# Optimization experiments

Hardware: AMD Instinct MI355X
Metric: run time of the kernel (lower is better)

Reference implementation:

```python
import jax, jax.numpy as jnp
import numpy as np

SEQ_LEN = 512
MAX_SPAN = 15
BATCH = 8
HIDDEN = 1024
WIDTH_DIM = 64
NUM_LABELS = 3


def _enumerate_spans(seq_len, max_span):
    starts, ends = [], []
    for s in range(seq_len):
        for e in range(s, min(s + max_span, seq_len)):
            starts.append(s)
            ends.append(e)
    return np.asarray(starts, np.int32), np.asarray(ends, np.int32)


def setup_inputs() -> dict:
    key = jax.random.key(0)
    k = jax.random.split(key, 6)
    starts, ends = _enumerate_spans(SEQ_LEN, MAX_SPAN)  # N = 7575
    d_in = HIDDEN * 2 + WIDTH_DIM  # 2112
    return {
        "sequence_output": jax.random.normal(k[0], (BATCH, SEQ_LEN, HIDDEN), jnp.float32),
        "width_emb": jax.random.normal(k[1], (MAX_SPAN, WIDTH_DIM), jnp.float32) * 0.02,
        "W1": jax.random.normal(k[2], (d_in, HIDDEN), jnp.float32) * (1.0 / np.sqrt(d_in)),
        "b1": jnp.zeros((HIDDEN,), jnp.float32),
        "W2": jax.random.normal(k[3], (HIDDEN, NUM_LABELS), jnp.float32) * (1.0 / np.sqrt(HIDDEN)),
        "b2": jnp.zeros((NUM_LABELS,), jnp.float32),
        "span_starts": jnp.asarray(starts),
        "span_ends": jnp.asarray(ends),
    }


def reference(sequence_output, width_emb, W1, b1, W2, b2, span_starts, span_ends):
    # Gather start/end token representations for every candidate span.
    B = sequence_output.shape[0]
    N = span_starts.shape[0]
    start_repr = sequence_output[:, span_starts]            # [B, N, H]
    end_repr = sequence_output[:, span_ends]                # [B, N, H]
    width_repr = width_emb[span_ends - span_starts]         # [N, 64]
    width_repr = jnp.broadcast_to(width_repr[None], (B, N, width_repr.shape[-1]))
    span_reprs = jnp.concatenate([start_repr, end_repr, width_repr], axis=-1)  # [B, N, 2H+64]
    # Span classifier MLP (dropout is identity in eval mode).
    h = jax.nn.relu(jnp.einsum("bnd,dh->bnh", span_reprs, W1) + b1)
    logits = jnp.einsum("bnh,hl->bnl", h, W2) + b2          # [B, N, num_labels]
    return logits
```

## Files before the change

### kernel.cpp

```cpp
#include <hip/hip_runtime.h>
#include <stdint.h>

#define SEQ 512
#define BATCH 8
#define HID 1024

typedef __attribute__((ext_vector_type(8))) __bf16 bf16x8;
typedef __attribute__((ext_vector_type(4))) float f32x4;
typedef __attribute__((ext_vector_type(2))) float f32x2;

__device__ __forceinline__ unsigned short f2bf(float f) {
    unsigned int u = __float_as_uint(f);
    unsigned int r = 0x7fffu + ((u >> 16) & 1u);
    return (unsigned short)((u + r) >> 16);
}

__device__ __forceinline__ f32x2 up2(unsigned int v) {
    f32x2 r;
    r.x = __uint_as_float(v << 16);
    r.y = __uint_as_float(v & 0xffff0000u);
    return r;
}

template <int CTRL>
__device__ __forceinline__ float dpp_add(float x) {
    int t = __builtin_amdgcn_update_dpp(0, __float_as_int(x), CTRL, 0xf, 0xf, true);
    return x + __int_as_float(t);
}
__device__ __forceinline__ float wave_sum63(float x) {
    x = dpp_add<0x111>(x);
    x = dpp_add<0x112>(x);
    x = dpp_add<0x114>(x);
    x = dpp_add<0x118>(x);
    x = dpp_add<0x142>(x);
    x = dpp_add<0x143>(x);
    return x;
}

__global__ __launch_bounds__(256) void k_prep(const float* __restrict__ seq,
                                              const float* __restrict__ W1,
                                              ushort* __restrict__ seqb,
                                              ushort* __restrict__ Bt) {
    __shared__ float tile[32][33];
    const int bid = blockIdx.x;
    const int tid = threadIdx.x;
    if (bid < 4096) {
        int i = bid * 256 + tid;
        float4 v = ((const float4*)seq)[i];
        ushort4 o;
        o.x = f2bf(v.x); o.y = f2bf(v.y); o.z = f2bf(v.z); o.w = f2bf(v.w);
        ((ushort4*)seqb)[i] = o;
    } else {
        int idx = bid - 4096;
        int nb = (idx & 63) * 32, kb = (idx >> 6) * 32;
        int tx = tid & 31, ty = tid >> 5;
        int n = nb + tx;
        int rb = (n < 1024) ? 0 : 1024;
        int nc = n - rb;
#pragma unroll
        for (int i = 0; i < 4; ++i) {
            int k = kb + ty + i * 8;
            tile[ty + i * 8][tx] = W1[(size_t)(rb + k) * 1024 + nc];
        }
        __syncthreads();
#pragma unroll
        for (int i = 0; i < 4; ++i) {
            int n2 = nb + ty + i * 8;
            Bt[(size_t)n2 * 1024 + kb + tx] = f2bf(tile[tx][ty + i * 8]);
        }
    }
}

__global__ __launch_bounds__(256) void k_gemm(const ushort* __restrict__ A,
                                              const ushort* __restrict__ Bt,
                                              const float* __restrict__ wemb,
                                              const float* __restrict__ W1,
                                              const float* __restrict__ b1,
                                              const float* __restrict__ W2,
                                              ushort* __restrict__ P,
                                              ushort* __restrict__ Q,
                                              float* __restrict__ Rf,
                                              float* __restrict__ W2t) {
    __shared__ ushort Al[2][8192];
    __shared__ ushort Bl[2][8192];
    const int tid = threadIdx.x;
    const int bid = blockIdx.x;
    if (bid >= 512) {
        if (bid < 572) {
            int idx = (bid - 512) * 256 + tid;
            int w = idx >> 10, j = idx & 1023;
            float a0 = b1[j], a1 = 0.f, a2 = 0.f, a3 = 0.f;
#pragma unroll
            for (int c = 0; c < 64; c += 4) {
                a0 = fmaf(wemb[w * 64 + c + 0], W1[(size_t)(2048 + c + 0) * 1024 + j], a0);
                a1 = fmaf(wemb[w * 64 + c + 1], W1[(size_t)(2048 + c + 1) * 1024 + j], a1);
                a2 = fmaf(wemb[w * 64 + c + 2], W1[(size_t)(2048 + c + 2) * 1024 + j], a2);
                a3 = fmaf(wemb[w * 64 + c + 3], W1[(size_t)(2048 + c + 3) * 1024 + j], a3);
            }
            Rf[idx] = (a0 + a1) + (a2 + a3);
        } else {
            int idx = (bid - 572) * 256 + tid;
            int l = idx >> 10, j = idx & 1023;
            W2t[idx] = W2[j * 3 + l];
        }
        return;
    }
    const int wid = tid >> 6;
    const int lane = tid & 63;
    const int x = bid & 7, t8 = bid >> 3;
    const int m0 = (((x >> 1) << 3) + (t8 >> 3)) * 128;
    const int n0 = (((x & 1) << 3) + (t8 & 7)) * 128;
    const int wm = (wid >> 1) * 64;
    const int wn = (wid & 1) * 64;
    const int srow = lane >> 2;
    const int scol = (lane & 3) * 8;
    const int fr = lane & 15;
    const int fk = (lane >> 4) * 8;

    f32x4 acc[4][4] = {};

    const ushort* Abase = A  + (size_t)(m0 + srow) * 1024 + scol;
    const ushort* Bbase = Bt + (size_t)(n0 + srow) * 1024 + scol;

#define STAGE(buf, k0)                                                                     \
    {                                                                                      \
        _Pragma("unroll")                                                                  \
        for (int r = 0; r < 4; ++r) {                                                      \
            int c = wid + 4 * r;                                                           \
            int half = c >> 3;                                                             \
            int rows = (c & 7) * 16;                                                       \
            const ushort* sa = Abase + (size_t)rows * 1024 + (k0) + half * 32;             \
            const ushort* sb = Bbase + (size_t)rows * 1024 + (k0) + half * 32;             \
            int loff = half * 4096 + rows * 32;                                            \
            __builtin_amdgcn_global_load_lds((const __attribute__((address_space(1))) void*)sa, \
                                             (__attribute__((address_space(3))) void*)(&Al[buf][loff]), \
                                             16, 0, 0);                                    \
            __builtin_amdgcn_global_load_lds((const __attribute__((address_space(1))) void*)sb, \
                                             (__attribute__((address_space(3))) void*)(&Bl[buf][loff]), \
                                             16, 0, 0);                                    \
        }                                                                                  \
    }

#define COMPUTE(cur)                                                                       \
    {                                                                                      \
        _Pragma("unroll")                                                                  \
        for (int kk = 0; kk < 2; ++kk) {                                                   \
            bf16x8 af[4], bg[4];                                                           \
            _Pragma("unroll")                                                              \
            for (int i = 0; i < 4; ++i)                                                    \
                af[i] = *(const bf16x8*)(&Al[cur][kk * 4096 + (wm + i * 16 + fr) * 32 + fk]); \
            _Pragma("unroll")                                                              \
            for (int j = 0; j < 4; ++j)                                                    \
                bg[j] = *(const bf16x8*)(&Bl[cur][kk * 4096 + (wn + j * 16 + fr) * 32 + fk]); \
            __builtin_amdgcn_s_setprio(1);                                                 \
            _Pragma("unroll")                                                              \
            for (int i = 0; i < 4; ++i)                                                    \
                _Pragma("unroll")                                                          \
                for (int j = 0; j < 4; ++j)                                                \
                    acc[i][j] = __builtin_amdgcn_mfma_f32_16x16x32_bf16(af[i], bg[j], acc[i][j], 0, 0, 0); \
            __builtin_amdgcn_s_setprio(0);                                                 \
        }                                                                                  \
    }

    STAGE(0, 0);
    for (int t = 0; t < 15; ++t) {
        const int cur = t & 1;
        STAGE(cur ^ 1, (t + 1) * 64);
        asm volatile("s_waitcnt vmcnt(8)" ::: "memory");
        __builtin_amdgcn_s_barrier();
        COMPUTE(cur);
        __builtin_amdgcn_s_barrier();
    }
    asm volatile("s_waitcnt vmcnt(0)" ::: "memory");
    __builtin_amdgcn_s_barrier();
    COMPUTE(1);
#undef STAGE
#undef COMPUTE

    ushort* Cb = (n0 < 1024) ? P : Q;
    const int nc0 = n0 & 1023;
    const int cr = (lane >> 4) * 4;
    const int cc = lane & 15;
#pragma unroll
    for (int i = 0; i < 4; ++i)
#pragma unroll
        for (int j = 0; j < 4; ++j) {
            ushort* Cp = Cb + (size_t)(m0 + wm + i * 16 + cr) * 1024 + (nc0 + wn + j * 16 + cc);
#pragma unroll
            for (int r = 0; r < 4; ++r)
                Cp[(size_t)r * 1024] = f2bf(acc[i][j][r]);
        }
}

__global__ __launch_bounds__(512, 2) void k_span9(const ushort* __restrict__ Pmat,
                                                  const ushort* __restrict__ Qmat,
                                                  const float* __restrict__ Rf,
                                                  const float* __restrict__ W2t,
                                                  const float* __restrict__ b2,
                                                  float* __restrict__ out, int nspans) {
    __shared__ float Rs[15 * 1024];
    const int tid = threadIdx.x;
    const int wid = tid >> 6, lane = tid & 63;
    const int b = blockIdx.x >> 6;
    const int s0 = (blockIdx.x & 63) << 3;

#pragma unroll
    for (int i = 0; i < 8; ++i) {
        int c = wid + (i << 3);
        if (c < 60) {
            int g = (c << 8) + lane * 4;
            __builtin_amdgcn_global_load_lds((const __attribute__((address_space(1))) void*)(Rf + g),
                                             (__attribute__((address_space(3))) void*)(Rs + g),
                                             16, 0, 0);
        }
    }

    f32x2 w2r2[3][2][4];
#pragma unroll
    for (int l = 0; l < 3; ++l)
#pragma unroll
        for (int it = 0; it < 2; ++it) {
            const float4* p = (const float4*)(W2t + l * 1024 + it * 512 + lane * 8);
            float4 v0 = p[0], v1 = p[1];
            w2r2[l][it][0] = (f32x2){v0.x, v0.y};
            w2r2[l][it][1] = (f32x2){v0.z, v0.w};
            w2r2[l][it][2] = (f32x2){v1.x, v1.y};
            w2r2[l][it][3] = (f32x2){v1.z, v1.w};
        }
    const float bb0 = b2[0], bb1 = b2[1], bb2 = b2[2];

    const int s = s0 + wid;
    f32x2 pf2[8];
    {
        const uint4* pr = (const uint4*)(Pmat + (((size_t)(b << 9) + s) << 10) + lane * 8);
        uint4 p0 = pr[0], p1 = pr[64];
        pf2[0] = up2(p0.x); pf2[1] = up2(p0.y); pf2[2] = up2(p0.z); pf2[3] = up2(p0.w);
        pf2[4] = up2(p1.x); pf2[5] = up2(p1.y); pf2[6] = up2(p1.z); pf2[7] = up2(p1.w);
    }

    __syncthreads();

    const int rrem = SEQ - s;
    const int nsp = (rrem < 15) ? rrem : 15;
    const int off = (rrem >= 15) ? 15 * s : (7575 - (rrem * (rrem + 1)) / 2);
    float* op = out + ((size_t)b * nspans + off) * 3;

    const uint4* qp = (const uint4*)(Qmat + (((size_t)(b << 9) + s) << 10) + lane * 8);

    int w = 0;
    for (; w + 1 < nsp; w += 2) {
        uint4 qa0 = qp[0],   qa1 = qp[64];
        uint4 qb0 = qp[128], qb1 = qp[192];
        qp += 256;
        f32x2 A0 = {0.f, 0.f}, A1 = {0.f, 0.f}, A2 = {0.f, 0.f};
        f32x2 B0 = {0.f, 0.f}, B1 = {0.f, 0.f}, B2 = {0.f, 0.f};
#pragma unroll
        for (int it = 0; it < 2; ++it) {
            uint4 qvA = it ? qa1 : qa0;
            uint4 qvB = it ? qb1 : qb0;
            const float4* rpA = (const float4*)(Rs + w * 1024 + it * 512 + lane * 8);
            const float4* rpB = (const float4*)(Rs + (w + 1) * 1024 + it * 512 + lane * 8);
            float4 raA = rpA[0], rbA = rpA[1];
            float4 raB = rpB[0], rbB = rpB[1];
            f32x2 q2A[4] = {up2(qvA.x), up2(qvA.y), up2(qvA.z), up2(qvA.w)};
            f32x2 q2B[4] = {up2(qvB.x), up2(qvB.y), up2(qvB.z), up2(qvB.w)};
            f32x2 r2A[4] = {(f32x2){raA.x, raA.y}, (f32x2){raA.z, raA.w},
                            (f32x2){rbA.x, rbA.y}, (f32x2){rbA.z, rbA.w}};
            f32x2 r2B[4] = {(f32x2){raB.x, raB.y}, (f32x2){raB.z, raB.w},
                            (f32x2){rbB.x, rbB.y}, (f32x2){rbB.z, rbB.w}};
#pragma unroll
            for (int k = 0; k < 4; ++k) {
                f32x2 hA = pf2[it * 4 + k] + q2A[k] + r2A[k];
                f32x2 hB = pf2[it * 4 + k] + q2B[k] + r2B[k];
                hA.x = fmaxf(hA.x, 0.f); hA.y = fmaxf(hA.y, 0.f);
                hB.x = fmaxf(hB.x, 0.f); hB.y = fmaxf(hB.y, 0.f);
                A0 += hA * w2r2[0][it][k];
                B0 += hB * w2r2[0][it][k];
                A1 += hA * w2r2[1][it][k];
                B1 += hB * w2r2[1][it][k];
                A2 += hA * w2r2[2][it][k];
                B2 += hB * w2r2[2][it][k];
            }
        }
        float a0 = A0.x + A0.y, b0 = B0.x + B0.y;
        float a1 = A1.x + A1.y, b1v = B1.x + B1.y;
        float a2 = A2.x + A2.y, b2v = B2.x + B2.y;
        a0 = wave_sum63(a0); b0 = wave_sum63(b0);
        a1 = wave_sum63(a1); b1v = wave_sum63(b1v);
        a2 = wave_sum63(a2); b2v = wave_sum63(b2v);
        if (lane == 63) {
            op[w * 3 + 0] = a0 + bb0;
            op[w * 3 + 1] = a1 + bb1;
            op[w * 3 + 2] = a2 + bb2;
            op[w * 3 + 3] = b0 + bb0;
            op[w * 3 + 4] = b1v + bb1;
            op[w * 3 + 5] = b2v + bb2;
        }
    }
    if (w < nsp) {
        uint4 qa0 = qp[0], qa1 = qp[64];
        f32x2 A0 = {0.f, 0.f}, A1 = {0.f, 0.f}, A2 = {0.f, 0.f};
#pragma unroll
        for (int it = 0; it < 2; ++it) {
            uint4 qv = it ? qa1 : qa0;
            const float4* rp = (const float4*)(Rs + w * 1024 + it * 512 + lane * 8);
            float4 ra = rp[0], rb = rp[1];
            f32x2 q2[4] = {up2(qv.x), up2(qv.y), up2(qv.z), up2(qv.w)};
            f32x2 r2[4] = {(f32x2){ra.x, ra.y}, (f32x2){ra.z, ra.w},
                           (f32x2){rb.x, rb.y}, (f32x2){rb.z, rb.w}};
#pragma unroll
            for (int k = 0; k < 4; ++k) {
                f32x2 h = pf2[it * 4 + k] + q2[k] + r2[k];
                h.x = fmaxf(h.x, 0.f); h.y = fmaxf(h.y, 0.f);
                A0 += h * w2r2[0][it][k];
                A1 += h * w2r2[1][it][k];
                A2 += h * w2r2[2][it][k];
            }
        }
        float a0 = A0.x + A0.y;
        float a1 = A1.x + A1.y;
        float a2 = A2.x + A2.y;
        a0 = wave_sum63(a0);
        a1 = wave_sum63(a1);
        a2 = wave_sum63(a2);
        if (lane == 63) {
            op[w * 3 + 0] = a0 + bb0;
            op[w * 3 + 1] = a1 + bb1;
            op[w * 3 + 2] = a2 + bb2;
        }
    }
}

extern "C" void kernel_launch(void* const* d_in, const int* in_sizes, int n_in,
                              void* d_out, int out_size, void* d_ws, size_t ws_size,
                              hipStream_t stream) {
    const float* seq    = (const float*)d_in[0];
    const float* wemb   = (const float*)d_in[1];
    const float* W1     = (const float*)d_in[2];
    const float* b1     = (const float*)d_in[3];
    const float* W2     = (const float*)d_in[4];
    const float* b2     = (const float*)d_in[5];
    float* out = (float*)d_out;
    int nspans = in_sizes[6];

    char* ws = (char*)d_ws;
    ushort* seqb = (ushort*)ws;
    ushort* Bt   = (ushort*)(ws + (8u << 20));
    ushort* Pmat = (ushort*)(ws + (12u << 20));
    ushort* Qmat = (ushort*)(ws + (20u << 20));
    float*  Rf   = (float*)(ws + (28u << 20));
    float*  W2t  = (float*)(ws + (29u << 20));

    hipLaunchKernelGGL(k_prep, dim3(6144), dim3(256), 0, stream, seq, W1, seqb, Bt);
    hipLaunchKernelGGL(k_gemm, dim3(584), dim3(256), 0, stream,
                       seqb, Bt, wemb, W1, b1, W2, Pmat, Qmat, Rf, W2t);
    hipLaunchKernelGGL(k_span9, dim3(BATCH * 64), dim3(512), 0, stream,
                       Pmat, Qmat, Rf, W2t, b2, out, nspans);
}
```

Before: 53.17 us.

## Restructure GEMM into 256x128 tiles with triple-buffered LDS and interleaved loads

The projection GEMM now uses 512-thread blocks computing 256x128 output tiles, halving the number of tiles. Staging moves to a three-stage LDS ring in dynamic shared memory, with the next-next K slice prefetched in pieces interleaved across four compute sub-steps. The intent is better latency hiding and more reuse of each B tile. It adds many more barriers per K step, needs 144KB of dynamic LDS per block (one block per CU), and fills fewer CUs with 256 GEMM blocks.

New measurement: 61.67 us. 1.16x slower.

```diff
diff --git a/kernel.cpp b/kernel.cpp
--- a/kernel.cpp
+++ b/kernel.cpp
@@ -71,23 +71,22 @@
     }
 }
 
-__global__ __launch_bounds__(256) void k_gemm(const ushort* __restrict__ A,
-                                              const ushort* __restrict__ Bt,
-                                              const float* __restrict__ wemb,
-                                              const float* __restrict__ W1,
-                                              const float* __restrict__ b1,
-                                              const float* __restrict__ W2,
-                                              ushort* __restrict__ P,
-                                              ushort* __restrict__ Q,
-                                              float* __restrict__ Rf,
-                                              float* __restrict__ W2t) {
-    __shared__ ushort Al[2][8192];
-    __shared__ ushort Bl[2][8192];
+__global__ __launch_bounds__(512) void k_gemm2(const ushort* __restrict__ A,
+                                               const ushort* __restrict__ Bt,
+                                               const float* __restrict__ wemb,
+                                               const float* __restrict__ W1,
+                                               const float* __restrict__ b1,
+                                               const float* __restrict__ W2,
+                                               ushort* __restrict__ P,
+                                               ushort* __restrict__ Q,
+                                               float* __restrict__ Rf,
+                                               float* __restrict__ W2t) {
+    extern __shared__ ushort sm[];
     const int tid = threadIdx.x;
     const int bid = blockIdx.x;
-    if (bid >= 512) {
-        if (bid < 572) {
-            int idx = (bid - 512) * 256 + tid;
+    if (bid >= 256) {
+        if (bid < 286) {
+            int idx = (bid - 256) * 512 + tid;
             int w = idx >> 10, j = idx & 1023;
             float a0 = b1[j], a1 = 0.f, a2 = 0.f, a3 = 0.f;
 #pragma unroll
@@ -99,7 +98,7 @@
             }
             Rf[idx] = (a0 + a1) + (a2 + a3);
         } else {
-            int idx = (bid - 572) * 256 + tid;
+            int idx = (bid - 286) * 512 + tid;
             int l = idx >> 10, j = idx & 1023;
             W2t[idx] = W2[j * 3 + l];
         }
@@ -107,9 +106,11 @@
     }
     const int wid = tid >> 6;
     const int lane = tid & 63;
-    const int x = bid & 7, t8 = bid >> 3;
-    const int m0 = (((x >> 1) << 3) + (t8 >> 3)) * 128;
-    const int n0 = (((x & 1) << 3) + (t8 & 7)) * 128;
+    const int x = bid & 7, tt = bid >> 3;
+    const int mt = ((x >> 1) << 2) + (tt >> 3);
+    const int nt = ((x & 1) << 3) + (tt & 7);
+    const int m0 = mt * 256;
+    const int n0 = nt * 128;
     const int wm = (wid >> 1) * 64;
     const int wn = (wid & 1) * 64;
     const int srow = lane >> 2;
@@ -119,63 +120,79 @@
 
     f32x4 acc[4][4] = {};
 
-    const ushort* Abase = A  + (size_t)(m0 + srow) * 1024 + scol;
-    const ushort* Bbase = Bt + (size_t)(n0 + srow) * 1024 + scol;
-
-#define STAGE(buf, k0)                                                                     \
+#define GLD(srcp, dstoff)                                                                  \
+    __builtin_amdgcn_global_load_lds((const __attribute__((address_space(1))) void*)(srcp), \
+                                     (__attribute__((address_space(3))) void*)(sm + (dstoff)), 16, 0, 0)
+#define STAGE_ALL(buf, k0)                                                                 \
     {                                                                                      \
-        _Pragma("unroll")                                                                  \
-        for (int r = 0; r < 4; ++r) {                                                      \
-            int c = wid + 4 * r;                                                           \
-            int half = c >> 3;                                                             \
-            int rows = (c & 7) * 16;                                                       \
-            const ushort* sa = Abase + (size_t)rows * 1024 + (k0) + half * 32;             \
-            const ushort* sb = Bbase + (size_t)rows * 1024 + (k0) + half * 32;             \
-            int loff = half * 4096 + rows * 32;                                            \
-            __builtin_amdgcn_global_load_lds((const __attribute__((address_space(1))) void*)sa, \
-                                             (__attribute__((address_space(3))) void*)(&Al[buf][loff]), \
-                                             16, 0, 0);                                    \
-            __builtin_amdgcn_global_load_lds((const __attribute__((address_space(1))) void*)sb, \
-                                             (__attribute__((address_space(3))) void*)(&Bl[buf][loff]), \
-                                             16, 0, 0);                                    \
-        }                                                                                  \
-    }
-
-#define COMPUTE(cur)                                                                       \
-    {                                                                                      \
-        _Pragma("unroll")                                                                  \
-        for (int kk = 0; kk < 2; ++kk) {                                                   \
-            bf16x8 af[4], bg[4];                                                           \
-            _Pragma("unroll")                                                              \
-            for (int i = 0; i < 4; ++i)                                                    \
-                af[i] = *(const bf16x8*)(&Al[cur][kk * 4096 + (wm + i * 16 + fr) * 32 + fk]); \
-            _Pragma("unroll")                                                              \
-            for (int j = 0; j < 4; ++j)                                                    \
-                bg[j] = *(const bf16x8*)(&Bl[cur][kk * 4096 + (wn + j * 16 + fr) * 32 + fk]); \
-            __builtin_amdgcn_s_setprio(1);                                                 \
-            _Pragma("unroll")                                                              \
-            for (int i = 0; i < 4; ++i)                                                    \
-                _Pragma("unroll")                                                          \
-                for (int j = 0; j < 4; ++j)                                                \
-                    acc[i][j] = __builtin_amdgcn_mfma_f32_16x16x32_bf16(af[i], bg[j], acc[i][j], 0, 0, 0); \
-            __builtin_amdgcn_s_setprio(0);                                                 \
-        }                                                                                  \
-    }
-
-    STAGE(0, 0);
-    for (int t = 0; t < 15; ++t) {
-        const int cur = t & 1;
-        STAGE(cur ^ 1, (t + 1) * 64);
-        asm volatile("s_waitcnt vmcnt(8)" ::: "memory");
-        __builtin_amdgcn_s_barrier();
-        COMPUTE(cur);
-        __builtin_amdgcn_s_barrier();
-    }
-    asm volatile("s_waitcnt vmcnt(0)" ::: "memory");
+        GLD(A  + (size_t)(m0 + wid * 16 + srow) * 1024 + (k0) + scol,        (buf) * 24576 + wid * 512);              \
+        GLD(A  + (size_t)(m0 + (wid + 8) * 16 + srow) * 1024 + (k0) + scol,  (buf) * 24576 + (wid + 8) * 512);        \
+        GLD(A  + (size_t)(m0 + wid * 16 + srow) * 1024 + (k0) + 32 + scol,       (buf) * 24576 + 8192 + wid * 512);   \
+        GLD(A  + (size_t)(m0 + (wid + 8) * 16 + srow) * 1024 + (k0) + 32 + scol, (buf) * 24576 + 8192 + (wid + 8) * 512); \
+        GLD(Bt + (size_t)(n0 + wid * 16 + srow) * 1024 + (k0) + scol,        (buf) * 24576 + 16384 + wid * 512);      \
+        GLD(Bt + (size_t)(n0 + wid * 16 + srow) * 1024 + (k0) + 32 + scol,   (buf) * 24576 + 16384 + 4096 + wid * 512); \
+    }
+
+    STAGE_ALL(0, 0);
+    STAGE_ALL(1, 64);
+    asm volatile("s_waitcnt vmcnt(6)" ::: "memory");
     __builtin_amdgcn_s_barrier();
-    COMPUTE(1);
-#undef STAGE
-#undef COMPUTE
+
+    for (int t = 0; t < 16; ++t) {
+        const int cur = t % 3;
+        const int nb = (t + 2) % 3;
+        const int k2 = (t + 2) * 64;
+        const bool st = (t < 14);
+        const ushort* base = sm + cur * 24576;
+#pragma unroll
+        for (int q = 0; q < 4; ++q) {
+            const int i0 = (q >> 1) * 2;
+            const int j0 = (q & 1) * 2;
+            bf16x8 aF[2][2], bF[2][2];
+#pragma unroll
+            for (int d = 0; d < 2; ++d)
+#pragma unroll
+                for (int kk = 0; kk < 2; ++kk) {
+                    aF[d][kk] = *(const bf16x8*)(base + kk * 8192 + (wm + (i0 + d) * 16 + fr) * 32 + fk);
+                    bF[d][kk] = *(const bf16x8*)(base + 16384 + kk * 4096 + (wn + (j0 + d) * 16 + fr) * 32 + fk);
+                }
+            if (st) {
+                if (q == 0) {
+                    GLD(A + (size_t)(m0 + wid * 16 + srow) * 1024 + k2 + scol,       nb * 24576 + wid * 512);
+                    GLD(A + (size_t)(m0 + (wid + 8) * 16 + srow) * 1024 + k2 + scol, nb * 24576 + (wid + 8) * 512);
+                } else if (q == 1) {
+                    GLD(A + (size_t)(m0 + wid * 16 + srow) * 1024 + k2 + 32 + scol,       nb * 24576 + 8192 + wid * 512);
+                    GLD(A + (size_t)(m0 + (wid + 8) * 16 + srow) * 1024 + k2 + 32 + scol, nb * 24576 + 8192 + (wid + 8) * 512);
+                } else if (q == 2) {
+                    GLD(Bt + (size_t)(n0 + wid * 16 + srow) * 1024 + k2 + scol, nb * 24576 + 16384 + wid * 512);
+                } else {
+                    GLD(Bt + (size_t)(n0 + wid * 16 + srow) * 1024 + k2 + 32 + scol, nb * 24576 + 16384 + 4096 + wid * 512);
+                }
+            }
+            __builtin_amdgcn_s_barrier();
+            asm volatile("s_waitcnt lgkmcnt(0)" ::: "memory");
+            __builtin_amdgcn_s_setprio(1);
+#pragma unroll
+            for (int kk = 0; kk < 2; ++kk)
+#pragma unroll
+                for (int di = 0; di < 2; ++di)
+#pragma unroll
+                    for (int dj = 0; dj < 2; ++dj)
+                        acc[i0 + di][j0 + dj] = __builtin_amdgcn_mfma_f32_16x16x32_bf16(
+                            aF[di][kk], bF[dj][kk], acc[i0 + di][j0 + dj], 0, 0, 0);
+            __builtin_amdgcn_s_setprio(0);
+            if (q == 3) {
+                if (t < 14) {
+                    asm volatile("s_waitcnt vmcnt(6)" ::: "memory");
+                } else if (t == 14) {
+                    asm volatile("s_waitcnt vmcnt(0)" ::: "memory");
+                }
+            }
+            __builtin_amdgcn_s_barrier();
+        }
+    }
+#undef STAGE_ALL
+#undef GLD
 
     ushort* Cb = (n0 < 1024) ? P : Q;
     const int nc0 = n0 & 1023;
@@ -351,8 +368,11 @@
     float*  Rf   = (float*)(ws + (28u << 20));
     float*  W2t  = (float*)(ws + (29u << 20));
 
+    hipFuncSetAttribute((const void*)k_gemm2,
+                        hipFuncAttributeMaxDynamicSharedMemorySize, 147456);
+
     hipLaunchKernelGGL(k_prep, dim3(6144), dim3(256), 0, stream, seq, W1, seqb, Bt);
-    hipLaunchKernelGGL(k_gemm, dim3(584), dim3(256), 0, stream,
+    hipLaunchKernelGGL(k_gemm2, dim3(292), dim3(512), 147456, stream,
                        seqb, Bt, wemb, W1, b1, W2, Pmat, Qmat, Rf, W2t);
     hipLaunchKernelGGL(k_span9, dim3(BATCH * 64), dim3(512), 0, stream,
                        Pmat, Qmat, Rf, W2t, b2, out, nspans);
```
